# Performance work log

Measured on AMD Instinct MI355X. Metric: run time of the kernel, lower is better.

## Reference

```python
import jax, jax.numpy as jnp
import numpy as np

DIM = 2048
HEADS = 16
HEAD_DIM = 128
B = 2
T = 2048


def _rope_as_in_source(x):
    # x: (b, h, t, d). FAITHFUL to the source bug: RotaryEmbedding uses
    # x.shape[1] (the HEADS axis, since it is called after transpose) as the
    # 'sequence' index, so rotation angle depends on head index and is
    # broadcast over the true sequence axis.
    n = x.shape[1]  # == heads
    d = x.shape[-1]
    inv_freq = 1.0 / (10000.0 ** (jnp.arange(0, d, 2, dtype=jnp.float32) / d))
    freqs = jnp.arange(n, dtype=jnp.float32)[:, None] * inv_freq[None, :]  # (h, d/2)
    cos = jnp.cos(freqs)[None, :, None, :]  # (1, h, 1, d/2)
    sin = jnp.sin(freqs)[None, :, None, :]
    x1 = x[..., 0::2]
    x2 = x[..., 1::2]
    out = jnp.stack([x1 * cos - x2 * sin, x1 * sin + x2 * cos], axis=-1)
    return out.reshape(x.shape)


def setup_inputs() -> dict:
    key = jax.random.key(0)
    ks = jax.random.split(key, 9)
    s_in = 1.0 / np.sqrt(DIM)
    hd = HEADS * HEAD_DIM
    s_o = 1.0 / np.sqrt(hd)
    return {
        "x": jax.random.normal(ks[0], (B, T, DIM), dtype=jnp.float32),
        "Wq": jax.random.normal(ks[1], (DIM, hd), dtype=jnp.float32) * s_in,
        "bq": jnp.zeros((hd,), dtype=jnp.float32),
        "Wk": jax.random.normal(ks[2], (DIM, hd), dtype=jnp.float32) * s_in,
        "bk": jnp.zeros((hd,), dtype=jnp.float32),
        "Wv": jax.random.normal(ks[3], (DIM, hd), dtype=jnp.float32) * s_in,
        "bv": jnp.zeros((hd,), dtype=jnp.float32),
        "Wo": jax.random.normal(ks[4], (hd, DIM), dtype=jnp.float32) * s_o,
        "bo": jnp.zeros((DIM,), dtype=jnp.float32),
    }


def reference(x, Wq, bq, Wk, bk, Wv, bv, Wo, bo):
    b, t, c = x.shape
    q = (x @ Wq + bq).reshape(b, t, HEADS, HEAD_DIM).transpose(0, 2, 1, 3)
    k = (x @ Wk + bk).reshape(b, t, HEADS, HEAD_DIM).transpose(0, 2, 1, 3)
    v = (x @ Wv + bv).reshape(b, t, HEADS, HEAD_DIM).transpose(0, 2, 1, 3)
    q = _rope_as_in_source(q)
    k = _rope_as_in_source(k)
    scale = 1.0 / np.sqrt(HEAD_DIM)
    scores = jnp.einsum("bhqd,bhkd->bhqk", q, k) * scale  # (b,h,t,t)
    attn = jax.nn.softmax(scores, axis=-1)
    out = jnp.einsum("bhqk,bhkd->bhqd", attn, v)  # (b,h,t,d)
    out = out.transpose(0, 2, 1, 3).reshape(b, t, HEADS * HEAD_DIM)
    return out @ Wo + bo
```

## Files before the change

### kernel.cpp

```cpp
#include <hip/hip_runtime.h>

typedef unsigned short ushort_t;
typedef unsigned int uint_t;
typedef __attribute__((ext_vector_type(8))) short short8;
typedef __attribute__((ext_vector_type(4))) float f32x4;
typedef __attribute__((ext_vector_type(4))) unsigned short ushort4_t;
typedef __attribute__((ext_vector_type(4))) unsigned int uint4_t;

__device__ inline ushort_t f2b(float f) {
    unsigned int x = __builtin_bit_cast(unsigned int, f);
    x += 0x7fffu + ((x >> 16) & 1u);
    return (ushort_t)(x >> 16);
}
__device__ inline uint_t cvt_pk_bf16(float lo, float hi) {
    uint_t r;
    asm("v_cvt_pk_bf16_f32 %0, %1, %2" : "=v"(r) : "v"(lo), "v"(hi));
    return r;
}

__device__ inline void gload16(const void* g, void* l) {
    __builtin_amdgcn_global_load_lds(
        (const __attribute__((address_space(1))) void*)g,
        (__attribute__((address_space(3))) void*)l, 16, 0, 0);
}

__device__ inline int xcd_swz512(int bid) {
    return (bid & 7) * 64 + (bid >> 3);
}

__global__ __launch_bounds__(256)
void cast_bf16(const float* __restrict__ src, ushort_t* __restrict__ dst) {
    size_t i = ((size_t)blockIdx.x * 256 + threadIdx.x) * 8;
    f32x4 a = *reinterpret_cast<const f32x4*>(src + i);
    f32x4 b = *reinterpret_cast<const f32x4*>(src + i + 4);
    short8 v;
#pragma unroll
    for (int j = 0; j < 4; ++j) { v[j] = (short)f2b(a[j]); v[4 + j] = (short)f2b(b[j]); }
    *reinterpret_cast<short8*>(dst + i) = v;
}

__global__ __launch_bounds__(64)
void transp4(const float* __restrict__ s0, const float* __restrict__ s1,
             const float* __restrict__ s2, const float* __restrict__ s3,
             ushort_t* __restrict__ d0, ushort_t* __restrict__ d1,
             ushort_t* __restrict__ d2, ushort_t* __restrict__ d3) {
    const int z = blockIdx.z;
    const float* src = (z == 0) ? s0 : (z == 1) ? s1 : (z == 2) ? s2 : s3;
    ushort_t* dst = (z == 0) ? d0 : (z == 1) ? d1 : (z == 2) ? d2 : d3;
    const int R = 2048, C = 2048;
    int r0 = blockIdx.x * 64 + ((threadIdx.x >> 3) << 3);
    int c0 = blockIdx.y * 64 + ((threadIdx.x & 7) << 3);
    ushort_t v[8][8];
#pragma unroll
    for (int i = 0; i < 8; ++i) {
        const float* p = src + (size_t)(r0 + i) * C + c0;
        f32x4 a = *reinterpret_cast<const f32x4*>(p);
        f32x4 b = *reinterpret_cast<const f32x4*>(p + 4);
#pragma unroll
        for (int j = 0; j < 4; ++j) { v[i][j] = f2b(a[j]); v[i][4 + j] = f2b(b[j]); }
    }
#pragma unroll
    for (int c = 0; c < 8; ++c) {
        short8 w;
#pragma unroll
        for (int i = 0; i < 8; ++i) w[i] = (short)v[i][c];
        *reinterpret_cast<short8*>(dst + (size_t)(c0 + c) * R + r0) = w;
    }
}

template <int MODE>
__global__ __launch_bounds__(256)
void gemm_qkv(const ushort_t* __restrict__ A, const ushort_t* __restrict__ Bt,
              const float* __restrict__ bias, ushort_t* __restrict__ C, float oscale) {
    const int K = 2048;
    __shared__ __align__(16) ushort_t As[128 * 64];
    __shared__ __align__(16) ushort_t Bs[128 * 64];
    const int tid = threadIdx.x, lane = tid & 63, wid = tid >> 6;
    const int l15 = lane & 15, g = lane >> 4;
    const int wr = wid >> 1, wc = wid & 1;
    const int lin = xcd_swz512(blockIdx.x);
    const int m0 = (lin >> 4) * 128, n0 = (lin & 15) * 128;
    f32x4 acc[4][4] = {};
    for (int k0 = 0; k0 < K; k0 += 64) {
#pragma unroll
        for (int is = 0; is < 4; ++is) {
            int c = is * 256 + tid;
            int row = c >> 3, sub = c & 7;
            int ks = (sub ^ (row & 7)) << 3;
            char* ldst = (char*)As + (size_t)(is * 256 + wid * 64) * 16;
            gload16(A + (size_t)(m0 + row) * K + k0 + ks, ldst);
            char* ldstB = (char*)Bs + (size_t)(is * 256 + wid * 64) * 16;
            gload16(Bt + (size_t)(n0 + row) * K + k0 + ks, ldstB);
        }
        __syncthreads();
#pragma unroll
        for (int kk = 0; kk < 2; ++kk) {
            short8 af[4], bf[4];
#pragma unroll
            for (int i = 0; i < 4; ++i) {
                int ra = wr * 64 + i * 16 + l15;
                af[i] = *reinterpret_cast<const short8*>(
                    (const char*)As + ra * 128 + (((4 * kk + g) ^ (ra & 7)) << 4));
                int rb = wc * 64 + i * 16 + l15;
                bf[i] = *reinterpret_cast<const short8*>(
                    (const char*)Bs + rb * 128 + (((4 * kk + g) ^ (rb & 7)) << 4));
            }
#pragma unroll
            for (int i = 0; i < 4; ++i)
#pragma unroll
                for (int j = 0; j < 4; ++j)
                    acc[i][j] = __builtin_amdgcn_mfma_f32_16x16x32_bf16(af[i], bf[j], acc[i][j], 0, 0, 0);
        }
        __syncthreads();
    }
#pragma unroll
    for (int j = 0; j < 4; ++j) {
        int n = n0 + wc * 64 + j * 16 + l15;
        float bj = bias[n];
        float sn = 0.f, cs = 1.f, sgn = 0.f;
        if (MODE == 0) {
            int d = n & 127, h = (n >> 7) & 15;
            float inv = expf(-(float)(d >> 1) * (9.210340371976184f / 64.0f));
            sincosf((float)h * inv, &sn, &cs);
            sgn = (d & 1) ? sn : -sn;
        }
#pragma unroll
        for (int i = 0; i < 4; ++i) {
            int mbase = m0 + wr * 64 + i * 16 + g * 4;
            if (MODE == 2) {
                int d = n & 127, hh = n >> 7;
                int b_ = mbase >> 11, t0 = mbase & 2047;
                ushort4_t w;
#pragma unroll
                for (int r = 0; r < 4; ++r) w[r] = f2b(acc[i][j][r] + bj);
                *reinterpret_cast<ushort4_t*>(
                    C + (((size_t)(b_ * 16 + hh) * 128 + d) * 2048 + t0)) = w;
            } else {
#pragma unroll
                for (int r = 0; r < 4; ++r) {
                    int m = mbase + r;
                    float v = acc[i][j][r] + bj;
                    float p = __shfl_xor(v, 1, 64);
                    v = fmaf(p, sgn, v * cs);
                    v *= oscale;
                    size_t addr = ((size_t)((m >> 11) * 16 + (n >> 7)) * 2048 + (m & 2047)) * 128 + (n & 127);
                    C[addr] = f2b(v);
                }
            }
        }
    }
}

__global__ __launch_bounds__(256)
void gemm_out(const ushort_t* __restrict__ A, const ushort_t* __restrict__ Bt,
              const float* __restrict__ bias, float* __restrict__ C,
              int M, int N, int K) {
    __shared__ __align__(16) ushort_t As[128 * 64];
    __shared__ __align__(16) ushort_t Bs[128 * 64];
    const int tid = threadIdx.x, lane = tid & 63, wid = tid >> 6;
    const int l15 = lane & 15, g = lane >> 4;
    const int wr = wid >> 1, wc = wid & 1;
    const int lin = xcd_swz512(blockIdx.x);
    const int m0 = (lin >> 4) * 128, n0 = (lin & 15) * 128;
    f32x4 acc[4][4] = {};
    for (int k0 = 0; k0 < K; k0 += 64) {
#pragma unroll
        for (int is = 0; is < 4; ++is) {
            int c = is * 256 + tid;
            int row = c >> 3, sub = c & 7;
            int ks = (sub ^ (row & 7)) << 3;
            char* ldst = (char*)As + (size_t)(is * 256 + wid * 64) * 16;
            gload16(A + (size_t)(m0 + row) * K + k0 + ks, ldst);
            char* ldstB = (char*)Bs + (size_t)(is * 256 + wid * 64) * 16;
            gload16(Bt + (size_t)(n0 + row) * K + k0 + ks, ldstB);
        }
        __syncthreads();
#pragma unroll
        for (int kk = 0; kk < 2; ++kk) {
            short8 af[4], bf[4];
#pragma unroll
            for (int i = 0; i < 4; ++i) {
                int ra = wr * 64 + i * 16 + l15;
                af[i] = *reinterpret_cast<const short8*>(
                    (const char*)As + ra * 128 + (((4 * kk + g) ^ (ra & 7)) << 4));
                int rb = wc * 64 + i * 16 + l15;
                bf[i] = *reinterpret_cast<const short8*>(
                    (const char*)Bs + rb * 128 + (((4 * kk + g) ^ (rb & 7)) << 4));
            }
#pragma unroll
            for (int i = 0; i < 4; ++i)
#pragma unroll
                for (int j = 0; j < 4; ++j)
                    acc[i][j] = __builtin_amdgcn_mfma_f32_16x16x32_bf16(af[i], bf[j], acc[i][j], 0, 0, 0);
        }
        __syncthreads();
    }
#pragma unroll
    for (int j = 0; j < 4; ++j) {
        int n = n0 + wc * 64 + j * 16 + l15;
        float bj = bias[n];
#pragma unroll
        for (int i = 0; i < 4; ++i) {
            int mbase = m0 + wr * 64 + i * 16 + g * 4;
#pragma unroll
            for (int r = 0; r < 4; ++r)
                C[(size_t)(mbase + r) * N + n] = acc[i][j][r] + bj;
        }
    }
}

__global__ __launch_bounds__(512)
void fattn(const ushort_t* __restrict__ Q, const ushort_t* __restrict__ K,
           const ushort_t* __restrict__ Vt, ushort_t* __restrict__ O) {
    __shared__ __align__(16) ushort_t Ks[2][64 * 128];
    __shared__ __align__(16) ushort_t Vs[2][128 * 64];
    const int tid = threadIdx.x, lane = tid & 63, wid = tid >> 6;
    const int l15 = lane & 15, g = lane >> 4;
    const int lin = xcd_swz512(blockIdx.x);
    const int qt = lin & 15, h = (lin >> 4) & 15, b = lin >> 8;
    const size_t base = ((size_t)b * 16 + h) * (2048 * 128);
    const int q0 = qt * 128 + wid * 16;
    const int q2 = l15 >> 2;
    const int sig = ((q2 == 1) ? 2 : (q2 == 2) ? 1 : q2) * 4 + (l15 & 3);
    short8 qf[4];
#pragma unroll
    for (int c = 0; c < 4; ++c)
        qf[c] = *reinterpret_cast<const short8*>(Q + base + (size_t)(q0 + l15) * 128 + c * 32 + g * 8);
    f32x4 oacc[8] = {};
    f32x4 oaccL = {};
    float m_r = -__builtin_inff();
    short8 ones;
#pragma unroll
    for (int j = 0; j < 8; ++j) ones[j] = (short)0x3F80;

    auto stage = [&](int kv0, int bsel) {
#pragma unroll
        for (int is = 0; is < 2; ++is) {
            {
                int c = is * 512 + tid;
                int row = c >> 4, sub = c & 15;
                int dsrc = (sub ^ (row & 7)) << 3;
                gload16(K + base + (size_t)(kv0 + row) * 128 + dsrc,
                        (char*)Ks[bsel] + (size_t)c * 16);
            }
            {
                int c = is * 512 + tid;
                int row = c >> 3, sub = c & 7;
                int tsrc = (sub ^ (row & 7)) << 3;
                gload16(Vt + base + (size_t)row * 2048 + kv0 + tsrc,
                        (char*)Vs[bsel] + (size_t)c * 16);
            }
        }
    };

    stage(0, 0);
    asm volatile("s_waitcnt vmcnt(0)" ::: "memory");
    __builtin_amdgcn_s_barrier();

    for (int it = 0; it < 32; ++it) {
        const int cur = it & 1;
        if (it < 31) stage((it + 1) << 6, cur ^ 1);
        f32x4 s[4] = {};
        __builtin_amdgcn_s_setprio(1);
#pragma unroll
        for (int nt = 0; nt < 4; ++nt) {
            int kvr = nt * 16 + sig;
#pragma unroll
            for (int c = 0; c < 4; ++c) {
                short8 kf = *reinterpret_cast<const short8*>(
                    (const char*)Ks[cur] + kvr * 256 + (((4 * c + g) ^ (sig & 7)) << 4));
                s[nt] = __builtin_amdgcn_mfma_f32_16x16x32_bf16(kf, qf[c], s[nt], 0, 0, 0);
            }
        }
        __builtin_amdgcn_s_setprio(0);
        float pm = fmaxf(fmaxf(fmaxf(s[0][0], s[0][1]), fmaxf(s[0][2], s[0][3])),
                         fmaxf(fmaxf(s[1][0], s[1][1]), fmaxf(s[1][2], s[1][3])));
        pm = fmaxf(pm, fmaxf(fmaxf(fmaxf(s[2][0], s[2][1]), fmaxf(s[2][2], s[2][3])),
                             fmaxf(fmaxf(s[3][0], s[3][1]), fmaxf(s[3][2], s[3][3]))));
        pm = fmaxf(pm, __shfl_xor(pm, 16, 64));
        pm = fmaxf(pm, __shfl_xor(pm, 32, 64));
        if (!__all(pm <= m_r + 5.0f)) {
            float mn = fmaxf(m_r, pm);
            float fac = exp2f(m_r - mn);
            m_r = mn;
#pragma unroll
            for (int r = 0; r < 4; ++r) oaccL[r] *= fac;
#pragma unroll
            for (int nt2 = 0; nt2 < 8; ++nt2)
#pragma unroll
                for (int r = 0; r < 4; ++r) oacc[nt2][r] *= fac;
        }
        uint_t W[4][2];
#pragma unroll
        for (int nt = 0; nt < 4; ++nt) {
            float p0 = exp2f(s[nt][0] - m_r);
            float p1 = exp2f(s[nt][1] - m_r);
            float p2 = exp2f(s[nt][2] - m_r);
            float p3 = exp2f(s[nt][3] - m_r);
            W[nt][0] = cvt_pk_bf16(p0, p1);
            W[nt][1] = cvt_pk_bf16(p2, p3);
        }
        __builtin_amdgcn_s_setprio(1);
#pragma unroll
        for (int ks = 0; ks < 2; ++ks) {
            uint_t A0 = W[2 * ks][0], A1 = W[2 * ks][1];
            uint_t B0 = W[2 * ks + 1][0], B1 = W[2 * ks + 1][1];
            asm("v_permlane32_swap_b32 %0, %1" : "+v"(A0), "+v"(B0));
            asm("v_permlane32_swap_b32 %0, %1" : "+v"(A1), "+v"(B1));
            uint4_t wv; wv[0] = A0; wv[1] = A1; wv[2] = B0; wv[3] = B1;
            short8 pb = __builtin_bit_cast(short8, wv);
            oaccL = __builtin_amdgcn_mfma_f32_16x16x32_bf16(ones, pb, oaccL, 0, 0, 0);
#pragma unroll
            for (int nt2 = 0; nt2 < 8; ++nt2) {
                int dr = nt2 * 16 + l15;
                short8 vb = *reinterpret_cast<const short8*>(
                    (const char*)Vs[cur] + dr * 128 + (((ks * 4 + g) ^ (dr & 7)) << 4));
                oacc[nt2] = __builtin_amdgcn_mfma_f32_16x16x32_bf16(vb, pb, oacc[nt2], 0, 0, 0);
            }
        }
        __builtin_amdgcn_s_setprio(0);
        asm volatile("s_waitcnt vmcnt(0)" ::: "memory");
        __builtin_amdgcn_s_barrier();
    }
    float inv = 1.f / oaccL[0];
    const size_t orow = ((size_t)b * 2048 + q0 + l15) * 2048 + (size_t)h * 128;
#pragma unroll
    for (int nt2 = 0; nt2 < 8; ++nt2) {
        ushort4_t w;
#pragma unroll
        for (int r = 0; r < 4; ++r) w[r] = f2b(oacc[nt2][r] * inv);
        *reinterpret_cast<ushort4_t*>(O + orow + nt2 * 16 + g * 4) = w;
    }
}

extern "C" void kernel_launch(void* const* d_in, const int* in_sizes, int n_in,
                              void* d_out, int out_size, void* d_ws, size_t ws_size,
                              hipStream_t stream) {
    const float* x  = (const float*)d_in[0];
    const float* Wq = (const float*)d_in[1];
    const float* bq = (const float*)d_in[2];
    const float* Wk = (const float*)d_in[3];
    const float* bk = (const float*)d_in[4];
    const float* Wv = (const float*)d_in[5];
    const float* bv = (const float*)d_in[6];
    const float* Wo = (const float*)d_in[7];
    const float* bo = (const float*)d_in[8];
    float* out = (float*)d_out;
    ushort_t* ws  = (ushort_t*)d_ws;

    const size_t WSZ = 2048ull * 2048;
    const size_t TSZ = 2ull * 16 * 2048 * 128;
    ushort_t* xb  = ws;
    ushort_t* Wtq = xb + TSZ;
    ushort_t* Wtk = Wtq + WSZ;
    ushort_t* Wtv = Wtk + WSZ;
    ushort_t* Wto = Wtv + WSZ;
    ushort_t* Qb  = Wto + WSZ;
    ushort_t* Kb  = Qb + TSZ;
    ushort_t* Vtb = Kb + TSZ;
    ushort_t* Sb  = Vtb + TSZ;

    const float QSC = 0.08838834764831845f * 1.4426950408889634f;

    cast_bf16<<<dim3(4096), 256, 0, stream>>>(x, xb);
    transp4<<<dim3(32, 32, 4), 64, 0, stream>>>(Wq, Wk, Wv, Wo, Wtq, Wtk, Wtv, Wto);

    gemm_qkv<0><<<dim3(512), 256, 0, stream>>>(xb, Wtq, bq, Qb, QSC);
    gemm_qkv<0><<<dim3(512), 256, 0, stream>>>(xb, Wtk, bk, Kb, 1.0f);
    gemm_qkv<2><<<dim3(512), 256, 0, stream>>>(xb, Wtv, bv, Vtb, 1.0f);

    fattn<<<dim3(512), 512, 0, stream>>>(Qb, Kb, Vtb, Sb);

    gemm_out<<<dim3(512), 256, 0, stream>>>(Sb, Wto, bo, out, 4096, 2048, 2048);
}
```

Before: 298.2 us.

## Process two 16-row query tiles per wave in flash attention to reuse K/V fragments

Each wave now handles 32 query rows (two 16-row MFMA tiles) instead of 16, so each block covers 256 queries and the grid halves to 256 blocks. Every K and V fragment read from LDS feeds two MFMAs, halving LDS reads and global K/V staging per query. The cost is doubled accumulator registers, which may lower occupancy, and only 256 blocks, which leaves some of the 256 CUs' worth of parallelism thin with no tail slack. The online-softmax rescale now fires when either tile's max grows.

Measured after the change: 300.9 us. No clear change (+0.9%).

```diff
diff --git a/kernel.cpp b/kernel.cpp
--- a/kernel.cpp
+++ b/kernel.cpp
@@ -26,6 +26,9 @@
 
 __device__ inline int xcd_swz512(int bid) {
     return (bid & 7) * 64 + (bid >> 3);
+}
+__device__ inline int xcd_swz256(int bid) {
+    return (bid & 7) * 32 + (bid >> 3);
 }
 
 __global__ __launch_bounds__(256)
@@ -216,19 +219,21 @@
     __shared__ __align__(16) ushort_t Vs[2][128 * 64];
     const int tid = threadIdx.x, lane = tid & 63, wid = tid >> 6;
     const int l15 = lane & 15, g = lane >> 4;
-    const int lin = xcd_swz512(blockIdx.x);
-    const int qt = lin & 15, h = (lin >> 4) & 15, b = lin >> 8;
+    const int lin = xcd_swz256(blockIdx.x);
+    const int qt = lin & 7, h = (lin >> 3) & 15, b = lin >> 7;
     const size_t base = ((size_t)b * 16 + h) * (2048 * 128);
-    const int q0 = qt * 128 + wid * 16;
+    const int q0 = qt * 256 + wid * 32;
     const int q2 = l15 >> 2;
     const int sig = ((q2 == 1) ? 2 : (q2 == 2) ? 1 : q2) * 4 + (l15 & 3);
-    short8 qf[4];
-#pragma unroll
-    for (int c = 0; c < 4; ++c)
-        qf[c] = *reinterpret_cast<const short8*>(Q + base + (size_t)(q0 + l15) * 128 + c * 32 + g * 8);
-    f32x4 oacc[8] = {};
-    f32x4 oaccL = {};
-    float m_r = -__builtin_inff();
+    short8 qfA[4], qfB[4];
+#pragma unroll
+    for (int c = 0; c < 4; ++c) {
+        qfA[c] = *reinterpret_cast<const short8*>(Q + base + (size_t)(q0 + l15) * 128 + c * 32 + g * 8);
+        qfB[c] = *reinterpret_cast<const short8*>(Q + base + (size_t)(q0 + 16 + l15) * 128 + c * 32 + g * 8);
+    }
+    f32x4 oaccA[8] = {}, oaccB[8] = {};
+    f32x4 oaccLA = {}, oaccLB = {};
+    float mA = -__builtin_inff(), mB = -__builtin_inff();
     short8 ones;
 #pragma unroll
     for (int j = 0; j < 8; ++j) ones[j] = (short)0x3F80;
@@ -260,7 +265,7 @@
     for (int it = 0; it < 32; ++it) {
         const int cur = it & 1;
         if (it < 31) stage((it + 1) << 6, cur ^ 1);
-        f32x4 s[4] = {};
+        f32x4 sA[4] = {}, sB[4] = {};
         __builtin_amdgcn_s_setprio(1);
 #pragma unroll
         for (int nt = 0; nt < 4; ++nt) {
@@ -269,67 +274,86 @@
             for (int c = 0; c < 4; ++c) {
                 short8 kf = *reinterpret_cast<const short8*>(
                     (const char*)Ks[cur] + kvr * 256 + (((4 * c + g) ^ (sig & 7)) << 4));
-                s[nt] = __builtin_amdgcn_mfma_f32_16x16x32_bf16(kf, qf[c], s[nt], 0, 0, 0);
+                sA[nt] = __builtin_amdgcn_mfma_f32_16x16x32_bf16(kf, qfA[c], sA[nt], 0, 0, 0);
+                sB[nt] = __builtin_amdgcn_mfma_f32_16x16x32_bf16(kf, qfB[c], sB[nt], 0, 0, 0);
             }
         }
         __builtin_amdgcn_s_setprio(0);
-        float pm = fmaxf(fmaxf(fmaxf(s[0][0], s[0][1]), fmaxf(s[0][2], s[0][3])),
-                         fmaxf(fmaxf(s[1][0], s[1][1]), fmaxf(s[1][2], s[1][3])));
-        pm = fmaxf(pm, fmaxf(fmaxf(fmaxf(s[2][0], s[2][1]), fmaxf(s[2][2], s[2][3])),
-                             fmaxf(fmaxf(s[3][0], s[3][1]), fmaxf(s[3][2], s[3][3]))));
-        pm = fmaxf(pm, __shfl_xor(pm, 16, 64));
-        pm = fmaxf(pm, __shfl_xor(pm, 32, 64));
-        if (!__all(pm <= m_r + 5.0f)) {
-            float mn = fmaxf(m_r, pm);
-            float fac = exp2f(m_r - mn);
-            m_r = mn;
-#pragma unroll
-            for (int r = 0; r < 4; ++r) oaccL[r] *= fac;
+        float pmA = fmaxf(fmaxf(fmaxf(sA[0][0], sA[0][1]), fmaxf(sA[0][2], sA[0][3])),
+                          fmaxf(fmaxf(sA[1][0], sA[1][1]), fmaxf(sA[1][2], sA[1][3])));
+        pmA = fmaxf(pmA, fmaxf(fmaxf(fmaxf(sA[2][0], sA[2][1]), fmaxf(sA[2][2], sA[2][3])),
+                               fmaxf(fmaxf(sA[3][0], sA[3][1]), fmaxf(sA[3][2], sA[3][3]))));
+        pmA = fmaxf(pmA, __shfl_xor(pmA, 16, 64));
+        pmA = fmaxf(pmA, __shfl_xor(pmA, 32, 64));
+        float pmB = fmaxf(fmaxf(fmaxf(sB[0][0], sB[0][1]), fmaxf(sB[0][2], sB[0][3])),
+                          fmaxf(fmaxf(sB[1][0], sB[1][1]), fmaxf(sB[1][2], sB[1][3])));
+        pmB = fmaxf(pmB, fmaxf(fmaxf(fmaxf(sB[2][0], sB[2][1]), fmaxf(sB[2][2], sB[2][3])),
+                               fmaxf(fmaxf(sB[3][0], sB[3][1]), fmaxf(sB[3][2], sB[3][3]))));
+        pmB = fmaxf(pmB, __shfl_xor(pmB, 16, 64));
+        pmB = fmaxf(pmB, __shfl_xor(pmB, 32, 64));
+        if (!__all(pmA <= mA + 5.0f && pmB <= mB + 5.0f)) {
+            float mnA = fmaxf(mA, pmA), mnB = fmaxf(mB, pmB);
+            float facA = exp2f(mA - mnA), facB = exp2f(mB - mnB);
+            mA = mnA; mB = mnB;
+#pragma unroll
+            for (int r = 0; r < 4; ++r) { oaccLA[r] *= facA; oaccLB[r] *= facB; }
 #pragma unroll
             for (int nt2 = 0; nt2 < 8; ++nt2)
 #pragma unroll
-                for (int r = 0; r < 4; ++r) oacc[nt2][r] *= fac;
-        }
-        uint_t W[4][2];
+                for (int r = 0; r < 4; ++r) { oaccA[nt2][r] *= facA; oaccB[nt2][r] *= facB; }
+        }
+        uint_t WA[4][2], WB[4][2];
 #pragma unroll
         for (int nt = 0; nt < 4; ++nt) {
-            float p0 = exp2f(s[nt][0] - m_r);
-            float p1 = exp2f(s[nt][1] - m_r);
-            float p2 = exp2f(s[nt][2] - m_r);
-            float p3 = exp2f(s[nt][3] - m_r);
-            W[nt][0] = cvt_pk_bf16(p0, p1);
-            W[nt][1] = cvt_pk_bf16(p2, p3);
+            WA[nt][0] = cvt_pk_bf16(exp2f(sA[nt][0] - mA), exp2f(sA[nt][1] - mA));
+            WA[nt][1] = cvt_pk_bf16(exp2f(sA[nt][2] - mA), exp2f(sA[nt][3] - mA));
+            WB[nt][0] = cvt_pk_bf16(exp2f(sB[nt][0] - mB), exp2f(sB[nt][1] - mB));
+            WB[nt][1] = cvt_pk_bf16(exp2f(sB[nt][2] - mB), exp2f(sB[nt][3] - mB));
         }
         __builtin_amdgcn_s_setprio(1);
 #pragma unroll
         for (int ks = 0; ks < 2; ++ks) {
-            uint_t A0 = W[2 * ks][0], A1 = W[2 * ks][1];
-            uint_t B0 = W[2 * ks + 1][0], B1 = W[2 * ks + 1][1];
+            uint_t A0 = WA[2 * ks][0], A1 = WA[2 * ks][1];
+            uint_t B0 = WA[2 * ks + 1][0], B1 = WA[2 * ks + 1][1];
             asm("v_permlane32_swap_b32 %0, %1" : "+v"(A0), "+v"(B0));
             asm("v_permlane32_swap_b32 %0, %1" : "+v"(A1), "+v"(B1));
-            uint4_t wv; wv[0] = A0; wv[1] = A1; wv[2] = B0; wv[3] = B1;
-            short8 pb = __builtin_bit_cast(short8, wv);
-            oaccL = __builtin_amdgcn_mfma_f32_16x16x32_bf16(ones, pb, oaccL, 0, 0, 0);
+            uint4_t wvA; wvA[0] = A0; wvA[1] = A1; wvA[2] = B0; wvA[3] = B1;
+            short8 pbA = __builtin_bit_cast(short8, wvA);
+            uint_t C0 = WB[2 * ks][0], C1 = WB[2 * ks][1];
+            uint_t D0 = WB[2 * ks + 1][0], D1 = WB[2 * ks + 1][1];
+            asm("v_permlane32_swap_b32 %0, %1" : "+v"(C0), "+v"(D0));
+            asm("v_permlane32_swap_b32 %0, %1" : "+v"(C1), "+v"(D1));
+            uint4_t wvB; wvB[0] = C0; wvB[1] = C1; wvB[2] = D0; wvB[3] = D1;
+            short8 pbB = __builtin_bit_cast(short8, wvB);
+            oaccLA = __builtin_amdgcn_mfma_f32_16x16x32_bf16(ones, pbA, oaccLA, 0, 0, 0);
+            oaccLB = __builtin_amdgcn_mfma_f32_16x16x32_bf16(ones, pbB, oaccLB, 0, 0, 0);
 #pragma unroll
             for (int nt2 = 0; nt2 < 8; ++nt2) {
                 int dr = nt2 * 16 + l15;
                 short8 vb = *reinterpret_cast<const short8*>(
                     (const char*)Vs[cur] + dr * 128 + (((ks * 4 + g) ^ (dr & 7)) << 4));
-                oacc[nt2] = __builtin_amdgcn_mfma_f32_16x16x32_bf16(vb, pb, oacc[nt2], 0, 0, 0);
+                oaccA[nt2] = __builtin_amdgcn_mfma_f32_16x16x32_bf16(vb, pbA, oaccA[nt2], 0, 0, 0);
+                oaccB[nt2] = __builtin_amdgcn_mfma_f32_16x16x32_bf16(vb, pbB, oaccB[nt2], 0, 0, 0);
             }
         }
         __builtin_amdgcn_s_setprio(0);
         asm volatile("s_waitcnt vmcnt(0)" ::: "memory");
         __builtin_amdgcn_s_barrier();
     }
-    float inv = 1.f / oaccL[0];
-    const size_t orow = ((size_t)b * 2048 + q0 + l15) * 2048 + (size_t)h * 128;
+    float invA = 1.f / oaccLA[0];
+    float invB = 1.f / oaccLB[0];
+    const size_t orowA = ((size_t)b * 2048 + q0 + l15) * 2048 + (size_t)h * 128;
+    const size_t orowB = ((size_t)b * 2048 + q0 + 16 + l15) * 2048 + (size_t)h * 128;
 #pragma unroll
     for (int nt2 = 0; nt2 < 8; ++nt2) {
-        ushort4_t w;
-#pragma unroll
-        for (int r = 0; r < 4; ++r) w[r] = f2b(oacc[nt2][r] * inv);
-        *reinterpret_cast<ushort4_t*>(O + orow + nt2 * 16 + g * 4) = w;
+        ushort4_t wA, wB;
+#pragma unroll
+        for (int r = 0; r < 4; ++r) {
+            wA[r] = f2b(oaccA[nt2][r] * invA);
+            wB[r] = f2b(oaccB[nt2][r] * invB);
+        }
+        *reinterpret_cast<ushort4_t*>(O + orowA + nt2 * 16 + g * 4) = wA;
+        *reinterpret_cast<ushort4_t*>(O + orowB + nt2 * 16 + g * 4) = wB;
     }
 }
 
@@ -369,7 +393,7 @@
     gemm_qkv<0><<<dim3(512), 256, 0, stream>>>(xb, Wtk, bk, Kb, 1.0f);
     gemm_qkv<2><<<dim3(512), 256, 0, stream>>>(xb, Wtv, bv, Vtb, 1.0f);
 
-    fattn<<<dim3(512), 512, 0, stream>>>(Qb, Kb, Vtb, Sb);
+    fattn<<<dim3(256), 512, 0, stream>>>(Qb, Kb, Vtb, Sb);
 
     gemm_out<<<dim3(512), 256, 0, stream>>>(Sb, Wto, bo, out, 4096, 2048, 2048);
 }
```
